# Kernel tuning notes

Hardware: AMD Instinct MI355X
Metric: run time of the kernel (lower is better)

The kernel has to match this reference:

```python
import jax, jax.numpy as jnp
import numpy as np

B, S, H = 64, 1024, 1024

def setup_inputs() -> dict:
    key = jax.random.key(0)
    k1, k2, k3, k4, k5 = jax.random.split(key, 5)
    scale = 1.0 / np.sqrt(H)
    return {
        "decoder_state": jax.random.normal(k1, (B, H), dtype=jnp.float32),
        "encoder_outputs": jax.random.normal(k2, (B, S, H), dtype=jnp.float32),
        "mask": jnp.ones((B, S), dtype=jnp.int32),
        "W_s": jax.random.uniform(k3, (H, H), minval=-scale, maxval=scale, dtype=jnp.float32),
        "W_h": jax.random.uniform(k4, (H, H), minval=-scale, maxval=scale, dtype=jnp.float32),
        "v": jax.random.uniform(k5, (H,), minval=-scale, maxval=scale, dtype=jnp.float32),
    }

def reference(decoder_state, encoder_outputs, mask, W_s, W_h, v):
    # Additive (Bahdanau) attention.
    # proj_s: [B, H] -- original applies W_s to the expanded state (same math, computed once)
    proj_s = decoder_state @ W_s.T
    # proj_h: [B, S, H]
    proj_h = jnp.einsum('bsh,kh->bsk', encoder_outputs, W_h)
    energy = jnp.tanh(proj_s[:, None, :] + proj_h)          # [B, S, H]
    scores = jnp.einsum('bsh,h->bs', energy, v)             # [B, S]
    scores = jnp.where(mask == 0, -jnp.inf, scores)
    weights = jax.nn.softmax(scores, axis=-1)               # [B, S]
    context = jnp.einsum('bs,bsh->bh', weights, encoder_outputs)  # [B, H]
    return context, weights
```

## Files before the change

kernel.cpp:

```cpp
#include <hip/hip_runtime.h>
#include <hip/hip_bf16.h>

#define B_ 64
#define S_ 1024
#define H_ 1024
#define M_ (B_*S_)

typedef __attribute__((ext_vector_type(8))) short short8;
typedef __attribute__((ext_vector_type(4))) float f32x4;

__device__ __forceinline__ unsigned short f2bf(float f) {
    union { float f; unsigned u; } c; c.f = f;
    unsigned u = c.u;
    unsigned r = (u + 0x7fffu + ((u >> 16) & 1u)) >> 16;
    return (unsigned short)r;
}

__device__ __forceinline__ float bf2f(unsigned short h) {
    union { unsigned u; float f; } c; c.u = ((unsigned)h) << 16;
    return c.f;
}

__device__ __forceinline__ float tanh_fast(float x) {
    float t = __expf(2.0f * x);
    return 1.0f - 2.0f * __builtin_amdgcn_rcpf(t + 1.0f);
}

__device__ __forceinline__ void gll16(const unsigned short* g, unsigned short* l) {
    auto* gp = (const __attribute__((address_space(1))) unsigned short*)(g);
    auto* lp = (__attribute__((address_space(3))) unsigned short*)(l);
    __builtin_amdgcn_global_load_lds(gp, lp, 16, 0, 0);
}

__global__ void cvt_bf16_kernel(const float* __restrict__ src,
                                unsigned short* __restrict__ dst, int n8) {
    int idx = blockIdx.x * blockDim.x + threadIdx.x;
    int stride = gridDim.x * blockDim.x;
    for (int i = idx; i < n8; i += stride) {
        const float4* s4 = (const float4*)src + (size_t)i * 2;
        float4 a = s4[0], b = s4[1];
        short8 o;
        o[0] = f2bf(a.x); o[1] = f2bf(a.y); o[2] = f2bf(a.z); o[3] = f2bf(a.w);
        o[4] = f2bf(b.x); o[5] = f2bf(b.y); o[6] = f2bf(b.z); o[7] = f2bf(b.w);
        *((short8*)dst + i) = o;
    }
}

__global__ void proj_s_part_kernel(const float* __restrict__ dec,
                                   const float* __restrict__ Ws,
                                   float* __restrict__ part) {
    __shared__ float wss[64][68];
    const int kt = blockIdx.x & 15, hs = blockIdx.x >> 4;
    const int k0 = kt * 64, h0 = hs * 64;
    const int t = threadIdx.x;

    {
        const int r = t >> 2, c = (t & 3) * 16;
        const float4* src = (const float4*)(Ws + (size_t)(k0 + r) * H_ + h0 + c);
        float4 v0 = src[0], v1 = src[1], v2 = src[2], v3 = src[3];
        *(float4*)&wss[r][c + 0]  = v0;
        *(float4*)&wss[r][c + 4]  = v1;
        *(float4*)&wss[r][c + 8]  = v2;
        *(float4*)&wss[r][c + 12] = v3;
    }
    const int b = t >> 2, kq = t & 3;
    float4 dreg[16];
    const float4* dsrc = (const float4*)(dec + (size_t)b * H_ + h0);
#pragma unroll
    for (int i = 0; i < 16; ++i) dreg[i] = dsrc[i];
    __syncthreads();

    float acc[16] = {};
#pragma unroll
    for (int h4 = 0; h4 < 16; ++h4) {
        float4 d = dreg[h4];
#pragma unroll
        for (int j = 0; j < 16; ++j) {
            float4 wv = *(const float4*)&wss[kq + 4 * j][h4 * 4];
            acc[j] = fmaf(d.x, wv.x, acc[j]);
            acc[j] = fmaf(d.y, wv.y, acc[j]);
            acc[j] = fmaf(d.z, wv.z, acc[j]);
            acc[j] = fmaf(d.w, wv.w, acc[j]);
        }
    }
#pragma unroll
    for (int j = 0; j < 16; ++j)
        part[(size_t)hs * M_ + b * H_ + k0 + kq + 4 * j] = acc[j];
}

__global__ void proj_red_kernel(const float* __restrict__ part,
                                float* __restrict__ proj_s) {
    int i = blockIdx.x * 256 + threadIdx.x;
    float s = 0.0f;
#pragma unroll
    for (int p = 0; p < 16; ++p) s += part[(size_t)p * M_ + i];
    proj_s[i] = s;
}

__global__ void __launch_bounds__(512)
fused_scores_8p_kernel(const unsigned short* __restrict__ encb,
                       const unsigned short* __restrict__ Whb,
                       const float* __restrict__ proj_s,
                       const float* __restrict__ v,
                       float* __restrict__ scores_part) {
    __shared__ __align__(16) unsigned short Lsh[32768];

    const int bx0 = blockIdx.x;
    const int bx = (bx0 & 7) * 128 + (bx0 >> 3);
    const int nt = bx & 3;
    const int mt = bx >> 2;
    const int t = threadIdx.x;
    const int wid = t >> 6, lane = t & 63;
    const int wr = wid >> 2, wc = wid & 3;
    const int lrow = lane & 15, lgrp = lane >> 4;

    f32x4 acc[8][4] = {};

    const int srow = t >> 2;
    const int scol = ((t & 3) ^ ((t >> 3) & 3)) * 8;
    const unsigned short* gA = encb + (size_t)(mt * 256 + srow) * H_ + scol;
    const unsigned short* gB = Whb  + (size_t)(nt * 256 + srow) * H_ + scol;
    unsigned short* lws = Lsh + wid * 512;

    #define STAGE(c, op, h, kt) \
        gll16(((op) ? gB : gA) + (size_t)(h) * (128 * H_) + (kt) * 32, \
              lws + (c) * 16384 + (op) * 8192 + (h) * 4096)

    int aoff[8], boff[4];
#pragma unroll
    for (int m = 0; m < 8; ++m) {
        int row = wr * 128 + m * 16 + lrow;
        aoff[m] = row * 64 + ((lgrp ^ ((row >> 1) & 3)) * 16);
    }
#pragma unroll
    for (int n = 0; n < 4; ++n) {
        int row = wc * 64 + n * 16 + lrow;
        boff[n] = row * 64 + ((lgrp ^ ((row >> 1) & 3)) * 16);
    }

    STAGE(0, 0, 0, 0); STAGE(0, 0, 1, 0); STAGE(0, 1, 0, 0); STAGE(0, 1, 1, 0);
    STAGE(1, 0, 0, 1); STAGE(1, 0, 1, 1); STAGE(1, 1, 0, 1);
    asm volatile("s_waitcnt vmcnt(3)" ::: "memory");
    __builtin_amdgcn_sched_barrier(0);
    __builtin_amdgcn_s_barrier();

    int cur = 0;
    for (int kt = 0; kt < 32; ++kt) {
#pragma unroll
        for (int p = 0; p < 4; ++p) {
            const int qm = p >> 1, qn = p & 1;
            short8 af[4], bfr[2];
#pragma unroll
            for (int mm = 0; mm < 4; ++mm)
                af[mm] = *(const short8*)((const char*)Lsh + cur * 32768 + aoff[qm * 4 + mm]);
#pragma unroll
            for (int nn = 0; nn < 2; ++nn)
                bfr[nn] = *(const short8*)((const char*)Lsh + cur * 32768 + 16384 + boff[qn * 2 + nn]);
            if (p == 0 && kt + 1 < 32) { STAGE(cur ^ 1, 1, 1, kt + 1); }
            __builtin_amdgcn_s_barrier();
            __builtin_amdgcn_s_setprio(1);
#pragma unroll
            for (int mm = 0; mm < 4; ++mm)
#pragma unroll
                for (int nn = 0; nn < 2; ++nn)
                    acc[qm * 4 + mm][qn * 2 + nn] =
                        __builtin_amdgcn_mfma_f32_16x16x32_bf16(af[mm], bfr[nn],
                            acc[qm * 4 + mm][qn * 2 + nn], 0, 0, 0);
            __builtin_amdgcn_s_setprio(0);
            __builtin_amdgcn_s_barrier();
        }
        if (kt + 2 < 32) {
            STAGE(cur, 0, 0, kt + 2);
            STAGE(cur, 0, 1, kt + 2);
            STAGE(cur, 1, 0, kt + 2);
        }
        asm volatile("s_waitcnt vmcnt(3)" ::: "memory");
        __builtin_amdgcn_sched_barrier(0);
        __builtin_amdgcn_s_barrier();
        cur ^= 1;
    }
    #undef STAGE

    const int b = mt >> 2;
    float vv[4], ps[4];
#pragma unroll
    for (int n = 0; n < 4; ++n) {
        int col = nt * 256 + wc * 64 + n * 16 + lrow;
        vv[n] = v[col];
        ps[n] = proj_s[b * H_ + col];
    }
    float* sums = (float*)Lsh;
#pragma unroll
    for (int m = 0; m < 8; ++m) {
#pragma unroll
        for (int j = 0; j < 4; ++j) {
            float s = 0.0f;
#pragma unroll
            for (int n = 0; n < 4; ++n)
                s = fmaf(tanh_fast(acc[m][n][j] + ps[n]), vv[n], s);
            s += __shfl_xor(s, 1, 64);
            s += __shfl_xor(s, 2, 64);
            s += __shfl_xor(s, 4, 64);
            s += __shfl_xor(s, 8, 64);
            if (lrow == 0)
                sums[(wr * 128 + m * 16 + lgrp * 4 + j) * 4 + wc] = s;
        }
    }
    __syncthreads();
    if (t < 256) {
        float r = sums[t * 4 + 0] + sums[t * 4 + 1] + sums[t * 4 + 2] + sums[t * 4 + 3];
        scores_part[(size_t)nt * M_ + mt * 256 + t] = r;
    }
}

__global__ void fused_scores_kernel(const float* __restrict__ enc,
                                    const float* __restrict__ Wh,
                                    const float* __restrict__ proj_s,
                                    const float* __restrict__ v,
                                    float* __restrict__ scores_part) {
    __shared__ __align__(16) unsigned short As[128][40];
    __shared__ __align__(16) unsigned short Bs[128][40];
    __shared__ float sums[128][2];

    const int bx = blockIdx.x;
    const int nt = bx & 7;
    const int mt = bx >> 3;
    const int t = threadIdx.x;
    const int w = t >> 6, lane = t & 63;
    const int wr = w >> 1, wc = w & 1;
    const int lrow = lane & 15, lgrp = lane >> 4;

    f32x4 acc[4][4] = {};

    const int srow = t >> 1;
    const int shalf = t & 1;
    const float* gA = enc + (size_t)(mt * 128 + srow) * H_ + shalf * 16;
    const float* gB = Wh  + (size_t)(nt * 128 + srow) * H_ + shalf * 16;
    unsigned short* lA = &As[srow][shalf * 16];
    unsigned short* lB = &Bs[srow][shalf * 16];

    for (int kt = 0; kt < H_ / 32; ++kt) {
        __syncthreads();
        const float4* a4 = (const float4*)(gA + kt * 32);
        const float4* b4 = (const float4*)(gB + kt * 32);
        union { unsigned short us[16]; uint4 q[2]; } pa, pb;
#pragma unroll
        for (int i = 0; i < 4; ++i) {
            float4 av = a4[i];
            float4 bv = b4[i];
            pa.us[i*4+0] = f2bf(av.x); pa.us[i*4+1] = f2bf(av.y);
            pa.us[i*4+2] = f2bf(av.z); pa.us[i*4+3] = f2bf(av.w);
            pb.us[i*4+0] = f2bf(bv.x); pb.us[i*4+1] = f2bf(bv.y);
            pb.us[i*4+2] = f2bf(bv.z); pb.us[i*4+3] = f2bf(bv.w);
        }
        *(uint4*)(lA)     = pa.q[0];
        *(uint4*)(lA + 8) = pa.q[1];
        *(uint4*)(lB)     = pb.q[0];
        *(uint4*)(lB + 8) = pb.q[1];
        __syncthreads();

        short8 af[4], bf[4];
#pragma unroll
        for (int m = 0; m < 4; ++m)
            af[m] = *(const short8*)&As[wr * 64 + m * 16 + lrow][lgrp * 8];
#pragma unroll
        for (int n = 0; n < 4; ++n)
            bf[n] = *(const short8*)&Bs[wc * 64 + n * 16 + lrow][lgrp * 8];
#pragma unroll
        for (int m = 0; m < 4; ++m)
#pragma unroll
            for (int n = 0; n < 4; ++n)
                acc[m][n] = __builtin_amdgcn_mfma_f32_16x16x32_bf16(af[m], bf[n], acc[m][n], 0, 0, 0);
    }

    const int b = mt >> 3;
    float vv[4], ps[4];
#pragma unroll
    for (int n = 0; n < 4; ++n) {
        int col = nt * 128 + wc * 64 + n * 16 + lrow;
        vv[n] = v[col];
        ps[n] = proj_s[b * H_ + col];
    }
    float rs[4][4];
#pragma unroll
    for (int m = 0; m < 4; ++m) {
#pragma unroll
        for (int j = 0; j < 4; ++j) {
            float s = 0.0f;
#pragma unroll
            for (int n = 0; n < 4; ++n)
                s = fmaf(tanh_fast(acc[m][n][j] + ps[n]), vv[n], s);
            s += __shfl_xor(s, 1, 64);
            s += __shfl_xor(s, 2, 64);
            s += __shfl_xor(s, 4, 64);
            s += __shfl_xor(s, 8, 64);
            rs[m][j] = s;
        }
    }
    if (lrow == 0) {
#pragma unroll
        for (int m = 0; m < 4; ++m)
#pragma unroll
            for (int j = 0; j < 4; ++j)
                sums[wr * 64 + m * 16 + lgrp * 4 + j][wc] = rs[m][j];
    }
    __syncthreads();
    if (t < 128)
        scores_part[(size_t)nt * M_ + mt * 128 + t] = sums[t][0] + sums[t][1];
}

__global__ void softmax_kernel(const float* __restrict__ scores_part,
                               const int* __restrict__ mask,
                               float* __restrict__ weights, int np) {
    const int b = blockIdx.x, t = threadIdx.x;
    __shared__ float red[8];
    float sc[4];
#pragma unroll
    for (int i = 0; i < 4; ++i) {
        int s = t + i * 256;
        float x = 0.0f;
        for (int p = 0; p < np; ++p)
            x += scores_part[(size_t)p * M_ + b * S_ + s];
        if (mask[b * S_ + s] == 0) x = -INFINITY;
        sc[i] = x;
    }
    float mx = fmaxf(fmaxf(sc[0], sc[1]), fmaxf(sc[2], sc[3]));
#pragma unroll
    for (int m = 32; m >= 1; m >>= 1) mx = fmaxf(mx, __shfl_xor(mx, m, 64));
    if ((t & 63) == 0) red[t >> 6] = mx;
    __syncthreads();
    mx = fmaxf(fmaxf(red[0], red[1]), fmaxf(red[2], red[3]));

    float e[4]; float sum = 0.0f;
#pragma unroll
    for (int i = 0; i < 4; ++i) { e[i] = __expf(sc[i] - mx); sum += e[i]; }
#pragma unroll
    for (int m = 32; m >= 1; m >>= 1) sum += __shfl_xor(sum, m, 64);
    if ((t & 63) == 0) red[4 + (t >> 6)] = sum;
    __syncthreads();
    sum = red[4] + red[5] + red[6] + red[7];
    float inv = 1.0f / sum;
#pragma unroll
    for (int i = 0; i < 4; ++i)
        weights[b * S_ + t + i * 256] = e[i] * inv;
}

__global__ void context_part_bf16_kernel(const unsigned short* __restrict__ encb,
                                         const float* __restrict__ weights,
                                         float* __restrict__ ctx_part) {
    const int b = blockIdx.x >> 5;
    const int sc = blockIdx.x & 31;
    const int t = threadIdx.x;
    __shared__ float wv[32];
    if (t < 32) wv[t] = weights[b * S_ + sc * 32 + t];
    __syncthreads();
    const short8* e8 = (const short8*)(encb + (size_t)(b * S_ + sc * 32) * H_) + t;
    float a[8] = {};
#pragma unroll 4
    for (int i = 0; i < 32; ++i) {
        short8 ev = e8[(size_t)i * 128];
        float w = wv[i];
#pragma unroll
        for (int j = 0; j < 8; ++j)
            a[j] = fmaf(w, bf2f((unsigned short)ev[j]), a[j]);
    }
    float* dst = ctx_part + (size_t)sc * M_ + b * H_ + t * 8;
    float4 o0; o0.x = a[0]; o0.y = a[1]; o0.z = a[2]; o0.w = a[3];
    float4 o1; o1.x = a[4]; o1.y = a[5]; o1.z = a[6]; o1.w = a[7];
    *(float4*)dst = o0;
    *(float4*)(dst + 4) = o1;
}

__global__ void context_part_kernel(const float* __restrict__ enc,
                                    const float* __restrict__ weights,
                                    float* __restrict__ ctx_part) {
    const int b = blockIdx.x >> 4;
    const int sc = blockIdx.x & 15;
    const int t = threadIdx.x;
    __shared__ float wv[64];
    if (t < 64) wv[t] = weights[b * S_ + sc * 64 + t];
    __syncthreads();
    const float4* e4 = (const float4*)(enc + (size_t)(b * S_ + sc * 64) * H_) + t;
    float ax = 0.f, ay = 0.f, az = 0.f, aw = 0.f;
#pragma unroll 4
    for (int i = 0; i < 64; ++i) {
        float4 ev = e4[i * 256];
        float wgt = wv[i];
        ax = fmaf(wgt, ev.x, ax);
        ay = fmaf(wgt, ev.y, ay);
        az = fmaf(wgt, ev.z, az);
        aw = fmaf(wgt, ev.w, aw);
    }
    float4 o; o.x = ax; o.y = ay; o.z = az; o.w = aw;
    *((float4*)(ctx_part + (size_t)sc * M_ + b * H_) + t) = o;
}

__global__ void ctx_reduce_kernel(const float* __restrict__ ctx_part,
                                  float* __restrict__ ctx, int np) {
    int idx = blockIdx.x * 256 + threadIdx.x;
    float s = 0.0f;
    for (int p = 0; p < np; ++p) s += ctx_part[(size_t)p * M_ + idx];
    ctx[idx] = s;
}

extern "C" void kernel_launch(void* const* d_in, const int* in_sizes, int n_in,
                              void* d_out, int out_size, void* d_ws, size_t ws_size,
                              hipStream_t stream) {
    const float* dec  = (const float*)d_in[0];
    const float* enc  = (const float*)d_in[1];
    const int*   mask = (const int*)d_in[2];
    const float* Ws   = (const float*)d_in[3];
    const float* Wh   = (const float*)d_in[4];
    const float* v    = (const float*)d_in[5];

    float* out = (float*)d_out;

    float* proj_s      = (float*)d_ws;
    float* proj_part   = proj_s + M_;
    float* scores_part = proj_part + 16 * (size_t)M_;
    float* ctx_part    = scores_part + 8 * (size_t)M_;
    unsigned short* encb = (unsigned short*)(ctx_part + 32 * (size_t)M_);
    unsigned short* Whb  = encb + (size_t)B_ * S_ * H_;

    const size_t need_small = 4ull * (1 + 16 + 8 + 32) * M_;
    const size_t need_big   = need_small + 2ull * ((size_t)B_ * S_ * H_ + (size_t)H_ * H_);

    proj_s_part_kernel<<<256, 256, 0, stream>>>(dec, Ws, proj_part);
    proj_red_kernel<<<256, 256, 0, stream>>>(proj_part, proj_s);

    if (ws_size >= need_big) {
        cvt_bf16_kernel<<<2048, 256, 0, stream>>>(enc, encb, B_ * S_ * H_ / 8);
        cvt_bf16_kernel<<<512, 256, 0, stream>>>(Wh, Whb, H_ * H_ / 8);
        fused_scores_8p_kernel<<<1024, 512, 0, stream>>>(encb, Whb, proj_s, v, scores_part);
        softmax_kernel<<<64, 256, 0, stream>>>(scores_part, mask, out + M_, 4);
        context_part_bf16_kernel<<<2048, 128, 0, stream>>>(encb, out + M_, ctx_part);
        ctx_reduce_kernel<<<256, 256, 0, stream>>>(ctx_part, out, 32);
    } else {
        fused_scores_kernel<<<4096, 256, 0, stream>>>(enc, Wh, proj_s, v, scores_part);
        softmax_kernel<<<64, 256, 0, stream>>>(scores_part, mask, out + M_, 8);
        context_part_kernel<<<1024, 256, 0, stream>>>(enc, out + M_, ctx_part);
        ctx_reduce_kernel<<<256, 256, 0, stream>>>(ctx_part, out, 16);
    }
}
```

Before: 280.8 us.

## Triple-buffer LDS tiles and restructure GEMM main loop into two halves

Grows LDS from two to three K-tile buffers so global loads for tile s+2 are issued while tile s is consumed, replacing the old double-buffer scheme with its awkward partial-stage prefetch. The inner loop now runs two phases of 16 MFMAs each, reusing four B fragments across both A halves instead of four phases of 8. This cuts LDS reads of B and lengthens the prefetch distance. The cost is 96KB of LDS per block, which may lower occupancy, plus more registers held live.

```diff
diff --git a/kernel.cpp b/kernel.cpp
--- a/kernel.cpp
+++ b/kernel.cpp
@@ -103,7 +103,7 @@
                        const float* __restrict__ proj_s,
                        const float* __restrict__ v,
                        float* __restrict__ scores_part) {
-    __shared__ __align__(16) unsigned short Lsh[32768];
+    __shared__ __align__(16) unsigned short Lsh[49152];
 
     const int bx0 = blockIdx.x;
     const int bx = (bx0 & 7) * 128 + (bx0 >> 3);
@@ -120,11 +120,10 @@
     const int scol = ((t & 3) ^ ((t >> 3) & 3)) * 8;
     const unsigned short* gA = encb + (size_t)(mt * 256 + srow) * H_ + scol;
     const unsigned short* gB = Whb  + (size_t)(nt * 256 + srow) * H_ + scol;
-    unsigned short* lws = Lsh + wid * 512;
-
-    #define STAGE(c, op, h, kt) \
+
+    #define STAGE(bufb, op, h, kt) \
         gll16(((op) ? gB : gA) + (size_t)(h) * (128 * H_) + (kt) * 32, \
-              lws + (c) * 16384 + (op) * 8192 + (h) * 4096)
+              Lsh + (bufb) * 16384 + (op) * 8192 + (h) * 4096 + wid * 512)
 
     int aoff[8], boff[4];
 #pragma unroll
@@ -139,45 +138,56 @@
     }
 
     STAGE(0, 0, 0, 0); STAGE(0, 0, 1, 0); STAGE(0, 1, 0, 0); STAGE(0, 1, 1, 0);
-    STAGE(1, 0, 0, 1); STAGE(1, 0, 1, 1); STAGE(1, 1, 0, 1);
-    asm volatile("s_waitcnt vmcnt(3)" ::: "memory");
+    STAGE(1, 0, 0, 1); STAGE(1, 0, 1, 1); STAGE(1, 1, 0, 1); STAGE(1, 1, 1, 1);
+    asm volatile("s_waitcnt vmcnt(4)" ::: "memory");
     __builtin_amdgcn_sched_barrier(0);
     __builtin_amdgcn_s_barrier();
 
-    int cur = 0;
-    for (int kt = 0; kt < 32; ++kt) {
-#pragma unroll
-        for (int p = 0; p < 4; ++p) {
-            const int qm = p >> 1, qn = p & 1;
-            short8 af[4], bfr[2];
-#pragma unroll
-            for (int mm = 0; mm < 4; ++mm)
-                af[mm] = *(const short8*)((const char*)Lsh + cur * 32768 + aoff[qm * 4 + mm]);
-#pragma unroll
-            for (int nn = 0; nn < 2; ++nn)
-                bfr[nn] = *(const short8*)((const char*)Lsh + cur * 32768 + 16384 + boff[qn * 2 + nn]);
-            if (p == 0 && kt + 1 < 32) { STAGE(cur ^ 1, 1, 1, kt + 1); }
-            __builtin_amdgcn_s_barrier();
-            __builtin_amdgcn_s_setprio(1);
-#pragma unroll
-            for (int mm = 0; mm < 4; ++mm)
-#pragma unroll
-                for (int nn = 0; nn < 2; ++nn)
-                    acc[qm * 4 + mm][qn * 2 + nn] =
-                        __builtin_amdgcn_mfma_f32_16x16x32_bf16(af[mm], bfr[nn],
-                            acc[qm * 4 + mm][qn * 2 + nn], 0, 0, 0);
-            __builtin_amdgcn_s_setprio(0);
-            __builtin_amdgcn_s_barrier();
-        }
-        if (kt + 2 < 32) {
-            STAGE(cur, 0, 0, kt + 2);
-            STAGE(cur, 0, 1, kt + 2);
-            STAGE(cur, 1, 0, kt + 2);
-        }
-        asm volatile("s_waitcnt vmcnt(3)" ::: "memory");
+    int bc = 0, bn = 2;
+    for (int s = 0; s < 32; ++s) {
+        const char* LA = (const char*)Lsh + bc * 32768;
+        const char* LB = LA + 16384;
+        const bool st = (s < 30);
+
+        short8 af[4], bfr[4];
+#pragma unroll
+        for (int m = 0; m < 4; ++m)
+            af[m] = *(const short8*)(LA + aoff[m]);
+#pragma unroll
+        for (int n = 0; n < 4; ++n)
+            bfr[n] = *(const short8*)(LB + boff[n]);
+        if (st) { STAGE(bn, 0, 0, s + 2); STAGE(bn, 0, 1, s + 2); }
+        __builtin_amdgcn_s_barrier();
+        __builtin_amdgcn_s_setprio(1);
+#pragma unroll
+        for (int m = 0; m < 4; ++m)
+#pragma unroll
+            for (int n = 0; n < 4; ++n)
+                acc[m][n] = __builtin_amdgcn_mfma_f32_16x16x32_bf16(af[m], bfr[n], acc[m][n], 0, 0, 0);
+        __builtin_amdgcn_s_setprio(0);
+        __builtin_amdgcn_s_barrier();
+
+        short8 af2[4];
+#pragma unroll
+        for (int m = 0; m < 4; ++m)
+            af2[m] = *(const short8*)(LA + aoff[4 + m]);
+        if (st) { STAGE(bn, 1, 0, s + 2); STAGE(bn, 1, 1, s + 2); }
+        __builtin_amdgcn_s_barrier();
+        __builtin_amdgcn_s_setprio(1);
+#pragma unroll
+        for (int m = 0; m < 4; ++m)
+#pragma unroll
+            for (int n = 0; n < 4; ++n)
+                acc[4 + m][n] = __builtin_amdgcn_mfma_f32_16x16x32_bf16(af2[m], bfr[n], acc[4 + m][n], 0, 0, 0);
+        __builtin_amdgcn_s_setprio(0);
+        __builtin_amdgcn_s_barrier();
+
+        if (s <= 29) { asm volatile("s_waitcnt vmcnt(4)" ::: "memory"); }
+        else         { asm volatile("s_waitcnt vmcnt(0)" ::: "memory"); }
         __builtin_amdgcn_sched_barrier(0);
         __builtin_amdgcn_s_barrier();
-        cur ^= 1;
+        bc = (bc == 2) ? 0 : bc + 1;
+        bn = (bn == 2) ? 0 : bn + 1;
     }
     #undef STAGE
 
```

Result: faster. 270.1 us (-3.8%).
